# Optimization experiments

Measured on AMD Instinct MI355X. Metric: run time of the kernel, lower is better.

## Reference

```python
import jax, jax.numpy as jnp
import numpy as np
import math

B, T, C = 8, 1024, 512
H = 8
HD = C // H  # 64
MAX_REL = 64 + 4  # args.block_size + args.time_cond


def setup_inputs() -> dict:
    key = jax.random.key(0)
    ks = jax.random.split(key, 12)
    xavier = lambda k, shape: jax.random.uniform(
        k, shape, jnp.float32, -1.0, 1.0) * math.sqrt(6.0 / (shape[0] + shape[1]))
    return {
        "x": jax.random.normal(ks[0], (B, T, C), jnp.float32),
        "Wq": xavier(ks[1], (C, C)), "bq": jnp.zeros((C,), jnp.float32),
        "Wk": xavier(ks[2], (C, C)), "bk": jnp.zeros((C,), jnp.float32),
        "Wv": xavier(ks[3], (C, C)), "bv": jnp.zeros((C,), jnp.float32),
        "Wo": xavier(ks[4], (C, C)), "bo": jnp.zeros((C,), jnp.float32),
        "rel_k": xavier(ks[5], (2 * MAX_REL + 1, HD)),
        "rel_v": xavier(ks[6], (2 * MAX_REL + 1, HD)),
    }


def _rel_index(t):
    # clipped relative distance matrix, shifted to [0, 2*MAX_REL]
    r = jnp.arange(t)
    dist = jnp.clip(r[None, :] - r[:, None], -MAX_REL, MAX_REL)
    return dist + MAX_REL  # (T, T) int32


def reference(x, Wq, bq, Wk, bk, Wv, bv, Wo, bo, rel_k, rel_v):
    b, t, c = x.shape
    h, hd = H, HD
    q = x @ Wq + bq
    k = x @ Wk + bk
    v = x @ Wv + bv
    rq = q.reshape(b, t, h, hd).transpose(0, 2, 1, 3)  # (B,H,T,hd)
    rk = k.reshape(b, t, h, hd).transpose(0, 2, 1, 3)
    rv = v.reshape(b, t, h, hd).transpose(0, 2, 1, 3)

    idx = _rel_index(t)                 # (T,T)
    rk2 = rel_k[idx]                    # (T,T,hd)
    rv2 = rel_v[idx]                    # (T,T,hd)

    attn1 = jnp.einsum("bhqd,bhkd->bhqk", rq, rk)
    attn2 = jnp.einsum("bhqd,qkd->bhqk", rq, rk2)
    # NOTE: original scales by 1/sqrt(embed_dim) (k.size(-1) == C), not head_dim
    attn = jax.nn.softmax((attn1 + attn2) * (1.0 / math.sqrt(c)), axis=-1)

    w1 = jnp.einsum("bhqk,bhkd->bhqd", attn, rv)
    w2 = jnp.einsum("bhqk,qkd->bhqd", attn, rv2)
    out = (w1 + w2).transpose(0, 2, 1, 3).reshape(b, t, c)
    return out @ Wo + bo
```

## Files before the change

### kernel.cpp

```cpp
#include <hip/hip_runtime.h>
#include <stdint.h>

#define Bb 8
#define Tt 1024
#define Cc 512
#define Hh 8
#define HD 64
#define MREL 68
#define NR 137
#define NRP 160
#define A2S 168
#define SS  1032
#define SCALE 0.044194173824159216f

typedef unsigned short u16;
using u16x4  = __attribute__((ext_vector_type(4))) u16;
using u16x8  = __attribute__((ext_vector_type(8))) u16;
using f32x4  = __attribute__((ext_vector_type(4))) float;
using bf16x8 = __attribute__((ext_vector_type(8))) __bf16;

__device__ __forceinline__ u16 f2bf(float f) {
  uint32_t u = __builtin_bit_cast(uint32_t, f);
  u += 0x7FFF + ((u >> 16) & 1);
  return (u16)(u >> 16);
}
__device__ __forceinline__ float bf2f(u16 v) {
  return __builtin_bit_cast(float, (uint32_t)v << 16);
}
__device__ __forceinline__ bf16x8 as_bf8(u16x8 v) { return __builtin_bit_cast(bf16x8, v); }

#define MFMA16(a, b, c) __builtin_amdgcn_mfma_f32_16x16x32_bf16((a), (b), (c), 0, 0, 0)

__global__ __launch_bounds__(256) void relv_prep(
    const float* __restrict__ rel_v, u16* __restrict__ rvT)
{
  int i = blockIdx.x * 256 + threadIdx.x;
  if (i < HD * NRP) {
    int d = i / NRP, r = i - d * NRP;
    rvT[i] = (r < NR) ? f2bf(rel_v[r * HD + d]) : (u16)0;
  }
}

__global__ __launch_bounds__(256) void w_prep(
    const float* __restrict__ Wq, const float* __restrict__ Wk,
    const float* __restrict__ Wv, const float* __restrict__ Wo,
    u16* __restrict__ WqT, u16* __restrict__ WkT,
    u16* __restrict__ WvT, u16* __restrict__ WoT)
{
  const float* W = blockIdx.y == 0 ? Wq : blockIdx.y == 1 ? Wk
                  : blockIdx.y == 2 ? Wv : Wo;
  u16* WT = blockIdx.y == 0 ? WqT : blockIdx.y == 1 ? WkT
           : blockIdx.y == 2 ? WvT : WoT;
  int i = blockIdx.x * 256 + threadIdx.x;
  int n = i >> 7, k4 = (i & 127) * 4;
  u16x4 o;
  #pragma unroll
  for (int j = 0; j < 4; ++j) o[j] = f2bf(W[(size_t)(k4 + j) * Cc + n]);
  *(u16x4*)&WT[(size_t)n * Cc + k4] = o;
}

__global__ __launch_bounds__(256) void qkv_gemm(
    const float* __restrict__ x,
    const u16* __restrict__ WqT, const u16* __restrict__ WkT,
    const u16* __restrict__ WvT,
    const float* __restrict__ bq, const float* __restrict__ bk,
    const float* __restrict__ bv,
    u16* __restrict__ Qb, u16* __restrict__ Kb, u16* __restrict__ VTb)
{
  __shared__ u16 Xs[64][40];
  __shared__ u16 WTs[3][64][40];

  const u16* Wp[3] = {WqT, WkT, WvT};
  const float* bp[3] = {bq, bk, bv};

  const int tid = threadIdx.x;
  const int wv_ = tid >> 6;
  const int l   = tid & 63;
  const int lr  = l & 15, lg = l >> 4;
  const int m0  = blockIdx.x * 64;
  const int n0  = blockIdx.y * 64;
  const int srow = tid >> 2, scol = (tid & 3) * 8;

  f32x4 acc[3][4];
  #pragma unroll
  for (int a = 0; a < 3; ++a)
    #pragma unroll
    for (int b = 0; b < 4; ++b) acc[a][b] = (f32x4){0.f, 0.f, 0.f, 0.f};

  for (int k0 = 0; k0 < Cc; k0 += 32) {
    {
      const float* xp = x + (size_t)(m0 + srow) * Cc + k0 + scol;
      f32x4 v0 = *(const f32x4*)xp;
      f32x4 v1 = *(const f32x4*)(xp + 4);
      u16x8 o = {f2bf(v0[0]), f2bf(v0[1]), f2bf(v0[2]), f2bf(v0[3]),
                 f2bf(v1[0]), f2bf(v1[1]), f2bf(v1[2]), f2bf(v1[3])};
      *(u16x8*)&Xs[srow][scol] = o;
    }
    #pragma unroll
    for (int q3 = 0; q3 < 3; ++q3) {
      u16x8 w = *(const u16x8*)(Wp[q3] + (size_t)(n0 + srow) * Cc + k0 + scol);
      *(u16x8*)&WTs[q3][srow][scol] = w;
    }
    __syncthreads();

    bf16x8 a = as_bf8(*(const u16x8*)&Xs[wv_ * 16 + lr][lg * 8]);
    #pragma unroll
    for (int q3 = 0; q3 < 3; ++q3) {
      #pragma unroll
      for (int nt = 0; nt < 4; ++nt) {
        bf16x8 b = as_bf8(*(const u16x8*)&WTs[q3][nt * 16 + lr][lg * 8]);
        acc[q3][nt] = MFMA16(a, b, acc[q3][nt]);
      }
    }
    __syncthreads();
  }

  const int bidx = m0 >> 10;
  #pragma unroll
  for (int q3 = 0; q3 < 3; ++q3) {
    #pragma unroll
    for (int nt = 0; nt < 4; ++nt) {
      int n = n0 + nt * 16 + lr;
      int h = n >> 6, d = n & 63;
      float bias = bp[q3][n];
      #pragma unroll
      for (int i = 0; i < 4; ++i) {
        int m = m0 + wv_ * 16 + lg * 4 + i;
        int t = m & (Tt - 1);
        u16 o = f2bf(acc[q3][nt][i] + bias);
        size_t bh = (size_t)(bidx * Hh + h);
        if (q3 == 0)      Qb[(bh * Tt + t) * HD + d] = o;
        else if (q3 == 1) Kb[(bh * Tt + t) * HD + d] = o;
        else              VTb[(bh * HD + d) * Tt + t] = o;
      }
    }
  }
}

__global__ __launch_bounds__(256) void attn_kernel(
    const u16* __restrict__ Qb, const u16* __restrict__ Kb,
    const u16* __restrict__ VTb, const u16* __restrict__ rvT,
    const float* __restrict__ rel_k,
    u16* __restrict__ AO)
{
  __shared__ u16 P[16][SS];
  __shared__ u16 S2a2[16][A2S];
  __shared__ float red[2][4][16];
  __shared__ float rowrcp[16];

  const int tid = threadIdx.x;
  const int wv_ = tid >> 6, l = tid & 63;
  const int lr = l & 15, lg = l >> 4;
  const int q0 = blockIdx.x * 16;
  const int bh = blockIdx.y;
  const int bidx = bh >> 3, h = bh & 7;

  const u16* Qh = Qb  + (size_t)bh * Tt * HD;
  const u16* Kh = Kb  + (size_t)bh * Tt * HD;
  const u16* Vh = VTb + (size_t)bh * HD * Tt;

  bf16x8 aQ0 = as_bf8(*(const u16x8*)(Qh + (size_t)(q0 + lr) * HD + lg * 8));
  bf16x8 aQ1 = as_bf8(*(const u16x8*)(Qh + (size_t)(q0 + lr) * HD + 32 + lg * 8));

  for (int ct = wv_; ct < 9; ct += 4) {
    int r = ct * 16 + lr;
    f32x4 acc = {0.f, 0.f, 0.f, 0.f};
    #pragma unroll
    for (int d0 = 0; d0 < 64; d0 += 32) {
      u16x8 bbits = {0, 0, 0, 0, 0, 0, 0, 0};
      if (r < NR) {
        f32x4 v0 = *(const f32x4*)(rel_k + (size_t)r * HD + d0 + lg * 8);
        f32x4 v1 = *(const f32x4*)(rel_k + (size_t)r * HD + d0 + lg * 8 + 4);
        bbits = (u16x8){f2bf(v0[0]), f2bf(v0[1]), f2bf(v0[2]), f2bf(v0[3]),
                        f2bf(v1[0]), f2bf(v1[1]), f2bf(v1[2]), f2bf(v1[3])};
      }
      acc = MFMA16(d0 ? aQ1 : aQ0, as_bf8(bbits), acc);
    }
    #pragma unroll
    for (int i = 0; i < 4; ++i)
      S2a2[lg * 4 + i][ct * 16 + lr] = f2bf(acc[i] * SCALE);
  }
  __syncthreads();

  float ps[4]  = {0.f, 0.f, 0.f, 0.f};
  float ps0[4] = {0.f, 0.f, 0.f, 0.f};

  int ktA = (q0 >= 131) ? (((q0 - 131) >> 6) + 1) : 0;
  int ktB = (q0 >= 53)  ? (((q0 - 53)  >> 6) + 1) : 0;
  if (ktA > 16) ktA = 16;
  if (ktB > 16) ktB = 16;

  auto body = [&](int kt, int MODE) {
    int kc = kt * 64 + wv_ * 16 + lr;
    bf16x8 b0 = as_bf8(*(const u16x8*)(Kh + (size_t)kc * HD + lg * 8));
    bf16x8 b1 = as_bf8(*(const u16x8*)(Kh + (size_t)kc * HD + 32 + lg * 8));
    f32x4 acc = {0.f, 0.f, 0.f, 0.f};
    acc = MFMA16(aQ0, b0, acc);
    acc = MFMA16(aQ1, b1, acc);
    int b2 = kc - q0 - lg * 4;
    #pragma unroll
    for (int i = 0; i < 4; ++i) {
      int row = lg * 4 + i;
      int dr = b2 - i;
      dr = dr < -MREL ? -MREL : (dr > MREL ? MREL : dr);
      float p = __expf(fmaf(acc[i], SCALE, bf2f(S2a2[row][dr + MREL])));
      ps[i] += p;
      if (MODE == 2)      ps0[i] += p;
      else if (MODE == 1) { if (kc <= q0 + row - MREL) ps0[i] += p; }
      P[row][kc] = f2bf(p);
    }
  };
  for (int kt = 0;   kt < ktA; ++kt) body(kt, 2);
  for (int kt = ktA; kt < ktB; ++kt) body(kt, 1);
  for (int kt = ktB; kt < 16;  ++kt) body(kt, 0);

  #pragma unroll
  for (int off = 1; off < 16; off <<= 1) {
    #pragma unroll
    for (int i = 0; i < 4; ++i) {
      ps[i]  += __shfl_xor(ps[i], off);
      ps0[i] += __shfl_xor(ps0[i], off);
    }
  }
  if (lr == 0) {
    #pragma unroll
    for (int i = 0; i < 4; ++i) {
      red[0][wv_][lg * 4 + i] = ps[i];
      red[1][wv_][lg * 4 + i] = ps0[i];
    }
  }
  __syncthreads();

  {
    int row = tid >> 4, c16 = tid & 15;
    int qg = q0 + row;
    float band = 0.f;
    for (int r = 1 + c16; r < NR - 1; r += 16) {
      int k = qg + r - MREL;
      u16 v = (k >= 0 && k < Tt) ? P[row][k] : (u16)0;
      S2a2[row][r] = v;
      band += bf2f(v);
    }
    #pragma unroll
    for (int off = 1; off < 16; off <<= 1) band += __shfl_xor(band, off);
    for (int r = NR + c16; r < NRP; r += 16) S2a2[row][r] = 0;
    if (c16 == 0) {
      float t0 = red[0][0][row] + red[0][1][row] + red[0][2][row] + red[0][3][row];
      float t1 = red[1][0][row] + red[1][1][row] + red[1][2][row] + red[1][3][row];
      S2a2[row][0]      = f2bf(t1);
      S2a2[row][NR - 1] = f2bf(t0 - t1 - band);
      rowrcp[row] = 1.0f / t0;
    }
  }
  __syncthreads();

  f32x4 o = {0.f, 0.f, 0.f, 0.f};
  for (int k0 = 0; k0 < Tt; k0 += 32) {
    bf16x8 ap = as_bf8(*(const u16x8*)&P[lr][k0 + lg * 8]);
    bf16x8 bv = as_bf8(*(const u16x8*)(Vh + (size_t)(wv_ * 16 + lr) * Tt + k0 + lg * 8));
    o = MFMA16(ap, bv, o);
  }
  #pragma unroll
  for (int k0 = 0; k0 < NRP; k0 += 32) {
    bf16x8 aa = as_bf8(*(const u16x8*)&S2a2[lr][k0 + lg * 8]);
    bf16x8 br = as_bf8(*(const u16x8*)(rvT + (size_t)(wv_ * 16 + lr) * NRP + k0 + lg * 8));
    o = MFMA16(aa, br, o);
  }
  #pragma unroll
  for (int i = 0; i < 4; ++i) {
    int row = lg * 4 + i;
    float val = o[i] * rowrcp[row];
    int t = q0 + row, cc = h * HD + wv_ * 16 + lr;
    AO[((size_t)(bidx * Tt + t)) * Cc + cc] = f2bf(val);
  }
}

__global__ __launch_bounds__(256) void out_gemm(
    const u16* __restrict__ AO, const u16* __restrict__ WoT,
    const float* __restrict__ bo, float* __restrict__ out)
{
  __shared__ u16 As[64][40];
  __shared__ u16 WTs[64][40];
  const int tid = threadIdx.x;
  const int wv_ = tid >> 6, l = tid & 63, lr = l & 15, lg = l >> 4;
  const int m0 = blockIdx.x * 64, n0 = blockIdx.y * 64;
  const int srow = tid >> 2, scol = (tid & 3) * 8;

  f32x4 acc[4];
  #pragma unroll
  for (int b = 0; b < 4; ++b) acc[b] = (f32x4){0.f, 0.f, 0.f, 0.f};

  for (int k0 = 0; k0 < Cc; k0 += 32) {
    u16x8 av = *(const u16x8*)(AO + (size_t)(m0 + srow) * Cc + k0 + scol);
    *(u16x8*)&As[srow][scol] = av;
    u16x8 wv2 = *(const u16x8*)(WoT + (size_t)(n0 + srow) * Cc + k0 + scol);
    *(u16x8*)&WTs[srow][scol] = wv2;
    __syncthreads();

    bf16x8 a = as_bf8(*(const u16x8*)&As[wv_ * 16 + lr][lg * 8]);
    #pragma unroll
    for (int nt = 0; nt < 4; ++nt) {
      bf16x8 b = as_bf8(*(const u16x8*)&WTs[nt * 16 + lr][lg * 8]);
      acc[nt] = MFMA16(a, b, acc[nt]);
    }
    __syncthreads();
  }

  #pragma unroll
  for (int nt = 0; nt < 4; ++nt) {
    int n = n0 + nt * 16 + lr;
    float bias = bo[n];
    #pragma unroll
    for (int i = 0; i < 4; ++i) {
      int m = m0 + wv_ * 16 + lg * 4 + i;
      out[(size_t)m * Cc + n] = acc[nt][i] + bias;
    }
  }
}

extern "C" void kernel_launch(void* const* d_in, const int* in_sizes, int n_in,
                              void* d_out, int out_size, void* d_ws, size_t ws_size,
                              hipStream_t stream) {
  const float* x  = (const float*)d_in[0];
  const float* Wq = (const float*)d_in[1];
  const float* bq = (const float*)d_in[2];
  const float* Wk = (const float*)d_in[3];
  const float* bk = (const float*)d_in[4];
  const float* Wv = (const float*)d_in[5];
  const float* bv = (const float*)d_in[6];
  const float* Wo = (const float*)d_in[7];
  const float* bo = (const float*)d_in[8];
  const float* rk = (const float*)d_in[9];
  const float* rv = (const float*)d_in[10];

  const size_t BHTD = (size_t)Bb * Hh * Tt * HD;
  const size_t WSZ  = (size_t)Cc * Cc;

  u16* Qb = (u16*)d_out;
  u16* Kb = Qb + BHTD;
  u16* VT  = (u16*)d_ws;
  u16* AO  = VT + BHTD;
  u16* rvT = AO + BHTD;
  u16* WqT = rvT + (size_t)HD * NRP;
  u16* WkT = WqT + WSZ;
  u16* WvT = WkT + WSZ;
  u16* WoT = WvT + WSZ;
  float* outf = (float*)d_out;

  relv_prep<<<dim3((HD * NRP + 255) / 256), 256, 0, stream>>>(rv, rvT);
  w_prep<<<dim3(256, 4), 256, 0, stream>>>(Wq, Wk, Wv, Wo, WqT, WkT, WvT, WoT);
  qkv_gemm<<<dim3(128, 8), 256, 0, stream>>>(x, WqT, WkT, WvT, bq, bk, bv, Qb, Kb, VT);
  attn_kernel<<<dim3(64, 64), 256, 0, stream>>>(Qb, Kb, VT, rvT, rk, AO);
  out_gemm<<<dim3(128, 8), 256, 0, stream>>>(AO, WoT, bo, outf);
}
```

Measured before the change: 213.5 us.

## Use exp2 with prescaled logits, hoist clipped-bias constants, swizzle P in LDS

The softmax scale is folded together with log2(e) into a single constant, so the exponential becomes a raw v_exp_f32. The clipped relative-key bias for tiles lying entirely beyond the band is loaded once into registers instead of being indexed from LDS per element, and the band tile ranges are recomputed to match. The P buffer is stored with an XOR swizzle rather than padding, to reduce LDS bank conflicts on writes and MFMA reads. This adds risk if the tile bounds do not exactly cover the band, and bf16 rounding of the bias now happens in the log2 domain.

```diff
diff --git a/kernel.cpp b/kernel.cpp
--- a/kernel.cpp
+++ b/kernel.cpp
@@ -10,8 +10,8 @@
 #define NR 137
 #define NRP 160
 #define A2S 168
-#define SS  1032
 #define SCALE 0.044194173824159216f
+#define KSCL  0.063763016845703125f
 
 typedef unsigned short u16;
 using u16x4  = __attribute__((ext_vector_type(4))) u16;
@@ -28,8 +28,12 @@
   return __builtin_bit_cast(float, (uint32_t)v << 16);
 }
 __device__ __forceinline__ bf16x8 as_bf8(u16x8 v) { return __builtin_bit_cast(bf16x8, v); }
+__device__ __forceinline__ float fexp2(float x) {
+  float r; asm("v_exp_f32 %0, %1" : "=v"(r) : "v"(x)); return r;
+}
 
 #define MFMA16(a, b, c) __builtin_amdgcn_mfma_f32_16x16x32_bf16((a), (b), (c), 0, 0, 0)
+#define PSWZ(row, col) ((col) ^ (((row) & 7) << 3))
 
 __global__ __launch_bounds__(256) void relv_prep(
     const float* __restrict__ rel_v, u16* __restrict__ rvT)
@@ -143,7 +147,7 @@
     const float* __restrict__ rel_k,
     u16* __restrict__ AO)
 {
-  __shared__ u16 P[16][SS];
+  __shared__ u16 P[16][1024];
   __shared__ u16 S2a2[16][A2S];
   __shared__ float red[2][4][16];
   __shared__ float rowrcp[16];
@@ -178,17 +182,22 @@
     }
     #pragma unroll
     for (int i = 0; i < 4; ++i)
-      S2a2[lg * 4 + i][ct * 16 + lr] = f2bf(acc[i] * SCALE);
+      S2a2[lg * 4 + i][ct * 16 + lr] = f2bf(acc[i] * KSCL);
   }
   __syncthreads();
+
+  float cN[4], cP[4];
+  #pragma unroll
+  for (int i = 0; i < 4; ++i) {
+    cN[i] = bf2f(S2a2[lg * 4 + i][0]);
+    cP[i] = bf2f(S2a2[lg * 4 + i][NR - 1]);
+  }
+
+  int ktLo = q0 > 130 ? (q0 - 130 + 63) >> 6 : 0;
+  int ktHi = (q0 + 82) >> 6; if (ktHi > 15) ktHi = 15;
 
   float ps[4]  = {0.f, 0.f, 0.f, 0.f};
   float ps0[4] = {0.f, 0.f, 0.f, 0.f};
-
-  int ktA = (q0 >= 131) ? (((q0 - 131) >> 6) + 1) : 0;
-  int ktB = (q0 >= 53)  ? (((q0 - 53)  >> 6) + 1) : 0;
-  if (ktA > 16) ktA = 16;
-  if (ktB > 16) ktB = 16;
 
   auto body = [&](int kt, int MODE) {
     int kc = kt * 64 + wv_ * 16 + lr;
@@ -201,18 +210,24 @@
     #pragma unroll
     for (int i = 0; i < 4; ++i) {
       int row = lg * 4 + i;
-      int dr = b2 - i;
-      dr = dr < -MREL ? -MREL : (dr > MREL ? MREL : dr);
-      float p = __expf(fmaf(acc[i], SCALE, bf2f(S2a2[row][dr + MREL])));
+      float c;
+      if (MODE == 2)      c = cN[i];
+      else if (MODE == 0) c = cP[i];
+      else {
+        int dr = b2 - i;
+        dr = dr < -MREL ? -MREL : (dr > MREL ? MREL : dr);
+        c = bf2f(S2a2[row][dr + MREL]);
+      }
+      float p = fexp2(fmaf(acc[i], KSCL, c));
       ps[i] += p;
       if (MODE == 2)      ps0[i] += p;
       else if (MODE == 1) { if (kc <= q0 + row - MREL) ps0[i] += p; }
-      P[row][kc] = f2bf(p);
+      P[row][PSWZ(row, kc)] = f2bf(p);
     }
   };
-  for (int kt = 0;   kt < ktA; ++kt) body(kt, 2);
-  for (int kt = ktA; kt < ktB; ++kt) body(kt, 1);
-  for (int kt = ktB; kt < 16;  ++kt) body(kt, 0);
+  for (int kt = 0;        kt < ktLo;  ++kt) body(kt, 2);
+  for (int kt = ktLo;     kt <= ktHi; ++kt) body(kt, 1);
+  for (int kt = ktHi + 1; kt < 16;    ++kt) body(kt, 0);
 
   #pragma unroll
   for (int off = 1; off < 16; off <<= 1) {
@@ -237,7 +252,7 @@
     float band = 0.f;
     for (int r = 1 + c16; r < NR - 1; r += 16) {
       int k = qg + r - MREL;
-      u16 v = (k >= 0 && k < Tt) ? P[row][k] : (u16)0;
+      u16 v = (k >= 0 && k < Tt) ? P[row][PSWZ(row, k)] : (u16)0;
       S2a2[row][r] = v;
       band += bf2f(v);
     }
@@ -256,7 +271,7 @@
 
   f32x4 o = {0.f, 0.f, 0.f, 0.f};
   for (int k0 = 0; k0 < Tt; k0 += 32) {
-    bf16x8 ap = as_bf8(*(const u16x8*)&P[lr][k0 + lg * 8]);
+    bf16x8 ap = as_bf8(*(const u16x8*)&P[lr][PSWZ(lr, k0 + lg * 8)]);
     bf16x8 bv = as_bf8(*(const u16x8*)(Vh + (size_t)(wv_ * 16 + lr) * Tt + k0 + lg * 8));
     o = MFMA16(ap, bv, o);
   }
```

Measured after the change: 213.1 us. About the same (-0.2%).
